# Kernel optimization log

Measured on AMD Instinct MI355X. Metric: run time of the kernel, lower is better.

Reference implementation:

```python
import jax, jax.numpy as jnp
import numpy as np

BN_EPS = 1e-5

def conv1x1(w, b, x):
    # w: [O, C], b: [O], x: [B, C, H, W] -> [B, O, H, W]
    return jnp.einsum('oc,bchw->bohw', w, x) + b[None, :, None, None]

def setup_inputs() -> dict:
    key = jax.random.key(0)
    ks = jax.random.split(key, 11)
    C, inter = 256, 128
    B, H, W = 16, 64, 32
    s = 0.05
    return {
        'x': jax.random.normal(ks[0], (B, C, H, W), jnp.float32),
        'g_w': jax.random.normal(ks[1], (inter, C), jnp.float32) * s,
        'g_b': jax.random.normal(ks[2], (inter,), jnp.float32) * s,
        'theta_w': jax.random.normal(ks[3], (inter, C), jnp.float32) * s,
        'theta_b': jax.random.normal(ks[4], (inter,), jnp.float32) * s,
        'phi_w': jax.random.normal(ks[5], (inter, C), jnp.float32) * s,
        'phi_b': jax.random.normal(ks[6], (inter,), jnp.float32) * s,
        'W_w': jax.random.normal(ks[7], (C, inter), jnp.float32) * s,
        'W_b': jax.random.normal(ks[8], (C,), jnp.float32) * s,
        'bn_gamma': jax.random.normal(ks[9], (C,), jnp.float32) * s,
        'bn_beta': jax.random.normal(ks[10], (C,), jnp.float32) * s,
    }

def reference(x, g_w, g_b, theta_w, theta_b, phi_w, phi_b, W_w, W_b, bn_gamma, bn_beta):
    B, C, H, W = x.shape
    N = H * W
    inter = g_w.shape[0]
    # 1x1 conv projections, flattened to token sequences
    g_x = conv1x1(g_w, g_b, x).reshape(B, inter, N).transpose(0, 2, 1)        # [B, N, inter]
    theta_x = conv1x1(theta_w, theta_b, x).reshape(B, inter, N).transpose(0, 2, 1)  # [B, N, inter]
    phi_x = conv1x1(phi_w, phi_b, x).reshape(B, inter, N)                      # [B, inter, N]
    # non-local attention: f = theta @ phi / N, then y = f @ g
    f_div_c = jnp.einsum('bnd,bdm->bnm', theta_x, phi_x) / N                   # [B, N, N]
    y = jnp.einsum('bnm,bmd->bnd', f_div_c, g_x)                               # [B, N, inter]
    y = y.transpose(0, 2, 1).reshape(B, inter, H, W)
    # W: 1x1 conv + BatchNorm (training-mode batch statistics)
    z = conv1x1(W_w, W_b, y)                                                   # [B, C, H, W]
    mean = jnp.mean(z, axis=(0, 2, 3), keepdims=True)
    var = jnp.var(z, axis=(0, 2, 3), keepdims=True)
    z_hat = (z - mean) * jax.lax.rsqrt(var + BN_EPS)
    z_bn = z_hat * bn_gamma[None, :, None, None] + bn_beta[None, :, None, None]
    return z_bn + x
```

## Files before the change

kernel.cpp:

```cpp
#include <hip/hip_runtime.h>

typedef unsigned int uint;
typedef unsigned short ushort;
typedef __attribute__((ext_vector_type(8))) short bf16x8;
typedef __attribute__((ext_vector_type(4))) float f32x4;

#define BB 16
#define CC 256
#define II 128
#define NN 2048
#define BN_EPS 1e-5f

#define OFF_GPART 0
#define OFF_SPART 8388608
#define OFF_CP    8421376
#define OFF_STATP 8425472
#define OFF_STAT2 8556544
#define OFF_PT    8557056
#define OFF_R1    8557312
#define OFF_WGB   8557568
#define OFF_ALPHA 8557824
#define OFF_L1    8558080
#define OFF_R2    8562176
#define OFF_FEND  8566272
#define UGRAM 0
#define UE    1048576
#define UFT   1114112
#define USBF  1179648
#define UXT   2228224
#define UZ    10616832

static __device__ __forceinline__ ushort f2bf(float f) {
    uint u = __float_as_uint(f);
    return (ushort)((u + 0x7FFFu + ((u >> 16) & 1u)) >> 16);
}
static __device__ __forceinline__ uint pack2(float a, float b) {
    return (uint)f2bf(a) | ((uint)f2bf(b) << 16);
}
static __device__ __forceinline__ float bflo(uint w) { return __uint_as_float(w << 16); }
static __device__ __forceinline__ float bfhi(uint w) { return __uint_as_float(w & 0xFFFF0000u); }

#define MICRO_FMA(av, bv) \
    acc[0][0] += av.x * bv.x; acc[0][1] += av.x * bv.y; acc[0][2] += av.x * bv.z; acc[0][3] += av.x * bv.w; \
    acc[1][0] += av.y * bv.x; acc[1][1] += av.y * bv.y; acc[1][2] += av.y * bv.z; acc[1][3] += av.y * bv.w; \
    acc[2][0] += av.z * bv.x; acc[2][1] += av.z * bv.y; acc[2][2] += av.z * bv.z; acc[2][3] += av.z * bv.w; \
    acc[3][0] += av.w * bv.x; acc[3][1] += av.w * bv.y; acc[3][2] += av.w * bv.z; acc[3][3] += av.w * bv.w;

__global__ __launch_bounds__(256) void mega1(
    const float* __restrict__ x,
    const float* __restrict__ Ww, const float* __restrict__ Gw,
    const float* __restrict__ Pw, const float* __restrict__ Tw,
    const float* __restrict__ gb, const float* __restrict__ pb, const float* __restrict__ tb,
    float* __restrict__ gpart, float* __restrict__ sPart, ushort* __restrict__ xT,
    ushort* __restrict__ EBF, ushort* __restrict__ FT,
    float* __restrict__ pt, float* __restrict__ r1, float* __restrict__ wgb,
    float* __restrict__ alpha)
{
    __shared__ __align__(16) char smem[20480];
    const int bid = blockIdx.x;
    const int t = threadIdx.x;

    if (bid < 512) {
        ushort (*As)[40] = (ushort(*)[40])smem;
        ushort (*Bs)[40] = (ushort(*)[40])(smem + 10240);
        const int jt = bid & 1, it = (bid >> 1) & 1;
        const int z = bid >> 2;
        const int b = z >> 3, kc = z & 7;
        const int iBase = it * 128, jBase = jt * 128;
        const bool diag = (it == jt);
        const int arow = t >> 1, ah = t & 1;
        const float* aSrc = x + ((size_t)(b * CC + iBase + arow)) * NN + kc * 256 + ah * 16;
        const float* bSrc = x + ((size_t)(b * CC + jBase + arow)) * NN + kc * 256 + ah * 16;
        const int lane = t & 63, wid = t >> 6;
        const int mb = (wid >> 1) * 64, nb = (wid & 1) * 64;
        const int lm = lane & 15, q = lane >> 4;
        f32x4 acc[4][4] = {};
        float ssum = 0.f;

        for (int it16 = 0; it16 < 8; ++it16) {
            const float4* ap = (const float4*)(aSrc + it16 * 32);
            float4 a0 = ap[0], a1 = ap[1], a2 = ap[2], a3 = ap[3];
            uint4 pa0 = { pack2(a0.x,a0.y), pack2(a0.z,a0.w), pack2(a1.x,a1.y), pack2(a1.z,a1.w) };
            uint4 pa1 = { pack2(a2.x,a2.y), pack2(a2.z,a2.w), pack2(a3.x,a3.y), pack2(a3.z,a3.w) };
            *(uint4*)&As[arow][ah * 16]     = pa0;
            *(uint4*)&As[arow][ah * 16 + 8] = pa1;
            if (!diag) {
                const float4* bp = (const float4*)(bSrc + it16 * 32);
                float4 b0 = bp[0], b1 = bp[1], b2 = bp[2], b3 = bp[3];
                uint4 pb0 = { pack2(b0.x,b0.y), pack2(b0.z,b0.w), pack2(b1.x,b1.y), pack2(b1.z,b1.w) };
                uint4 pb1 = { pack2(b2.x,b2.y), pack2(b2.z,b2.w), pack2(b3.x,b3.y), pack2(b3.z,b3.w) };
                *(uint4*)&Bs[arow][ah * 16]     = pb0;
                *(uint4*)&Bs[arow][ah * 16 + 8] = pb1;
            }
            if (jt == 0) {
                ssum += a0.x+a0.y+a0.z+a0.w + a1.x+a1.y+a1.z+a1.w
                      + a2.x+a2.y+a2.z+a2.w + a3.x+a3.y+a3.z+a3.w;
            }
            __syncthreads();
            const ushort (*Bsel)[40] = diag ? (const ushort(*)[40])As : (const ushort(*)[40])Bs;
            bf16x8 af[4], bf[4];
            #pragma unroll
            for (int mt = 0; mt < 4; ++mt)
                af[mt] = *(const bf16x8*)&As[mb + mt * 16 + lm][q * 8];
            #pragma unroll
            for (int nt = 0; nt < 4; ++nt)
                bf[nt] = *(const bf16x8*)&Bsel[nb + nt * 16 + lm][q * 8];
            #pragma unroll
            for (int mt = 0; mt < 4; ++mt)
                #pragma unroll
                for (int nt = 0; nt < 4; ++nt)
                    acc[mt][nt] = __builtin_amdgcn_mfma_f32_16x16x32_bf16(af[mt], bf[nt], acc[mt][nt], 0, 0, 0);
            if (diag) {
                const int n_l = t & 31, cg = t >> 5;
                uint qv[8];
                #pragma unroll
                for (int i2 = 0; i2 < 8; ++i2) {
                    ushort lo = As[cg * 16 + 2*i2][n_l];
                    ushort hi = As[cg * 16 + 2*i2 + 1][n_l];
                    qv[i2] = (uint)lo | ((uint)hi << 16);
                }
                const int ng = kc * 256 + it16 * 32 + n_l;
                uint4* op = (uint4*)(xT + ((size_t)(b * NN + ng)) * CC + iBase + cg * 16);
                op[0] = make_uint4(qv[0], qv[1], qv[2], qv[3]);
                op[1] = make_uint4(qv[4], qv[5], qv[6], qv[7]);
            }
            __syncthreads();
        }
        float* gp = gpart + ((size_t)kc * BB + b) * CC * CC;
        #pragma unroll
        for (int mt = 0; mt < 4; ++mt)
            #pragma unroll
            for (int nt = 0; nt < 4; ++nt)
                #pragma unroll
                for (int r = 0; r < 4; ++r) {
                    const int gi = iBase + mb + mt * 16 + q * 4 + r;
                    const int gj = jBase + nb + nt * 16 + lm;
                    gp[(size_t)gi * CC + gj] = acc[mt][nt][r];
                }
        if (jt == 0) {
            const float so = __shfl_xor(ssum, 1);
            if ((t & 1) == 0)
                sPart[((size_t)kc * BB + b) * CC + iBase + arow] = ssum + so;
        }
        return;
    }

    const int bz = bid - 512;
    if (bz == 32) {
        float ptv = 0.f, r1v = 0.f, wgbv = 0.f;
        for (int d = 0; d < II; ++d) {
            ptv  += Pw[(size_t)d * CC + t] * tb[d];
            r1v  += Tw[(size_t)d * CC + t] * pb[d];
            wgbv += Ww[(size_t)t * II + d] * gb[d];
        }
        pt[t] = ptv; r1[t] = r1v; wgb[t] = wgbv;
        if (t == 0) {
            float al = 0.f;
            for (int d = 0; d < II; ++d) al += pb[d] * tb[d];
            alpha[0] = al;
        }
        return;
    }
    float (*As)[68] = (float(*)[68])smem;
    float (*Bs)[68] = (float(*)[68])(smem + 8704);
    const int a_r = t >> 2, a_k = (t & 3) * 8;
    const int b_n = t & 63, b_k = t >> 6;
    const int ty = t >> 4, tx = t & 15;
    float acc[4][4] = {};
    if (bz < 16) {
        const int cBase = (bz >> 2) * 64, iBase = (bz & 3) * 64;
        const float* ap0 = Ww + (size_t)(cBase + a_r) * II + a_k;
        const float* bp0 = Gw + iBase + b_n;
        for (int k0 = 0; k0 < II; k0 += 32) {
            #pragma unroll
            for (int j = 0; j < 8; ++j) As[a_k + j][a_r] = ap0[k0 + j];
            #pragma unroll
            for (int kk = 0; kk < 8; ++kk) {
                const int k = b_k + kk * 4;
                Bs[k][b_n] = bp0[(size_t)(k0 + k) * CC];
            }
            __syncthreads();
            #pragma unroll
            for (int k = 0; k < 32; ++k) {
                const float4 av = *(const float4*)&As[k][ty * 4];
                const float4 bv = *(const float4*)&Bs[k][tx * 4];
                MICRO_FMA(av, bv)
            }
            __syncthreads();
        }
        #pragma unroll
        for (int ii = 0; ii < 4; ++ii) {
            uint2 o = { pack2(acc[ii][0], acc[ii][1]), pack2(acc[ii][2], acc[ii][3]) };
            *(uint2*)&EBF[(size_t)(cBase + ty * 4 + ii) * CC + iBase + tx * 4] = o;
        }
    } else {
        const int zz = bz - 16;
        const int jBase = (zz >> 2) * 64, kBase = (zz & 3) * 64;
        const float* ap0 = Tw + jBase + b_n;
        const float* bp0 = Pw + kBase + b_n;
        for (int k0 = 0; k0 < II; k0 += 32) {
            #pragma unroll
            for (int kk = 0; kk < 8; ++kk) {
                const int k = b_k + kk * 4;
                As[k][b_n] = ap0[(size_t)(k0 + k) * CC];
                Bs[k][b_n] = bp0[(size_t)(k0 + k) * CC];
            }
            __syncthreads();
            #pragma unroll
            for (int k = 0; k < 32; ++k) {
                const float4 av = *(const float4*)&As[k][ty * 4];
                const float4 bv = *(const float4*)&Bs[k][tx * 4];
                MICRO_FMA(av, bv)
            }
            __syncthreads();
        }
        const float sc = 1.0f / (float)NN;
        #pragma unroll
        for (int ii = 0; ii < 4; ++ii) {
            uint2 o = { pack2(acc[ii][0]*sc, acc[ii][1]*sc), pack2(acc[ii][2]*sc, acc[ii][3]*sc) };
            *(uint2*)&FT[(size_t)(jBase + ty * 4 + ii) * CC + kBase + tx * 4] = o;
        }
    }
}

__global__ __launch_bounds__(256) void mega2(
    const float* __restrict__ gpart, const float* __restrict__ sPart,
    const ushort* __restrict__ EBF, const ushort* __restrict__ FT,
    const float* __restrict__ pt, const float* __restrict__ r1,
    const float* __restrict__ wgb, const float* __restrict__ alpha,
    ushort* __restrict__ GramBF,
    float* __restrict__ cprime, float* __restrict__ L1, float* __restrict__ R2)
{
    const int bid = blockIdx.x;
    const int t = threadIdx.x;
    if (bid < 1024) {
        const int i = bid * 256 + t;
        const size_t S = (size_t)BB * CC * CC / 4;
        const float4* p = (const float4*)gpart;
        float4 o = { 0.f, 0.f, 0.f, 0.f };
        #pragma unroll
        for (int k = 0; k < 8; ++k) {
            float4 v = p[i + (size_t)k * S];
            o.x += v.x; o.y += v.y; o.z += v.z; o.w += v.w;
        }
        uint2 pk = { pack2(o.x, o.y), pack2(o.z, o.w) };
        ((uint2*)GramBF)[i] = pk;
        return;
    }
    const int b = bid - 1024;
    __shared__ __align__(16) float sL[256], ptL[256], GptL[256], red[256];
    {
        float s = 0.f;
        #pragma unroll
        for (int kc = 0; kc < 8; ++kc) s += sPart[((size_t)kc * BB + b) * CC + t];
        sL[t] = s;
        ptL[t] = pt[t];
    }
    __syncthreads();
    red[t] = sL[t] * ptL[t];
    __syncthreads();
    for (int s = 128; s > 0; s >>= 1) {
        if (t < s) red[t] += red[t + s];
        __syncthreads();
    }
    const float spt = red[0];
    const int lane = t & 63, wv = t >> 6;
    {
        const float4 pt4 = *(const float4*)&ptL[lane * 4];
        for (int r = wv; r < 256; r += 4) {
            float a = 0.f;
            #pragma unroll
            for (int kc = 0; kc < 8; ++kc) {
                const float4 g = *(const float4*)&gpart[(((size_t)kc * BB + b) * CC + r) * CC + lane * 4];
                a += g.x * pt4.x + g.y * pt4.y + g.z * pt4.z + g.w * pt4.w;
            }
            #pragma unroll
            for (int m = 32; m > 0; m >>= 1) a += __shfl_xor(a, m);
            if (lane == 0) GptL[r] = a;
        }
    }
    __syncthreads();
    float es = 0.f, eg = 0.f;
    {
        const uint4* ep = (const uint4*)(EBF + (size_t)t * CC);
        #pragma unroll 4
        for (int kk = 0; kk < 32; ++kk) {
            uint4 v = ep[kk]; const int k = kk * 8;
            float e0=bflo(v.x),e1=bfhi(v.x),e2=bflo(v.y),e3=bfhi(v.y);
            float e4=bflo(v.z),e5=bfhi(v.z),e6=bflo(v.w),e7=bfhi(v.w);
            es += e0*sL[k]+e1*sL[k+1]+e2*sL[k+2]+e3*sL[k+3]+e4*sL[k+4]+e5*sL[k+5]+e6*sL[k+6]+e7*sL[k+7];
            eg += e0*GptL[k]+e1*GptL[k+1]+e2*GptL[k+2]+e3*GptL[k+3]+e4*GptL[k+4]+e5*GptL[k+5]+e6*GptL[k+6]+e7*GptL[k+7];
        }
    }
    float r2 = 0.f;
    {
        const uint4* fp = (const uint4*)(FT + (size_t)t * CC);
        #pragma unroll 4
        for (int kk = 0; kk < 32; ++kk) {
            uint4 v = fp[kk]; const int k = kk * 8;
            r2 += bflo(v.x)*sL[k]   + bfhi(v.x)*sL[k+1] + bflo(v.y)*sL[k+2] + bfhi(v.y)*sL[k+3]
                + bflo(v.z)*sL[k+4] + bfhi(v.z)*sL[k+5] + bflo(v.w)*sL[k+6] + bfhi(v.w)*sL[k+7];
        }
    }
    const float al = alpha[0];
    const float wg = wgb[t];
    cprime[b * CC + t] = (eg + al * es + spt * wg) / (float)NN + al * wg;
    L1[b * CC + t] = es / (float)NN;
    R2[b * CC + t] = r2 + r1[t];
}

__global__ __launch_bounds__(256) void sfused(
    const ushort* __restrict__ EBF, const ushort* __restrict__ GramBF,
    const ushort* __restrict__ FT,
    const float* __restrict__ r1, const float* __restrict__ R2,
    const float* __restrict__ L1, const float* __restrict__ wgb,
    ushort* __restrict__ Sbf)
{
    __shared__ ushort As[128][40];
    __shared__ ushort Bs[128][40];
    __shared__ ushort Qs[128][264];
    const int t = threadIdx.x;
    const int b = blockIdx.x >> 2;
    const int ct = (blockIdx.x >> 1) & 1, jt = blockIdx.x & 1;
    const int cBase = ct * 128, jBase = jt * 128;
    const int arow = t >> 1, ah = t & 1;
    const int lane = t & 63, wid = t >> 6;
    const int mb = (wid >> 1) * 64, nb = (wid & 1) * 64;
    const int lm = lane & 15, q = lane >> 4;
    const ushort* aSrc = EBF + (size_t)(cBase + arow) * CC + ah * 16;

    #pragma unroll
    for (int half = 0; half < 2; ++half) {
        const ushort* bSrc = GramBF + ((size_t)b * CC + half * 128 + arow) * CC + ah * 16;
        f32x4 acc[4][4] = {};
        for (int k0 = 0; k0 < CC; k0 += 32) {
            *(uint4*)&As[arow][ah * 16]     = ((const uint4*)(aSrc + k0))[0];
            *(uint4*)&As[arow][ah * 16 + 8] = ((const uint4*)(aSrc + k0))[1];
            *(uint4*)&Bs[arow][ah * 16]     = ((const uint4*)(bSrc + k0))[0];
            *(uint4*)&Bs[arow][ah * 16 + 8] = ((const uint4*)(bSrc + k0))[1];
            __syncthreads();
            bf16x8 af[4], bf[4];
            #pragma unroll
            for (int mt = 0; mt < 4; ++mt)
                af[mt] = *(const bf16x8*)&As[mb + mt * 16 + lm][q * 8];
            #pragma unroll
            for (int nt = 0; nt < 4; ++nt)
                bf[nt] = *(const bf16x8*)&Bs[nb + nt * 16 + lm][q * 8];
            #pragma unroll
            for (int mt = 0; mt < 4; ++mt)
                #pragma unroll
                for (int nt = 0; nt < 4; ++nt)
                    acc[mt][nt] = __builtin_amdgcn_mfma_f32_16x16x32_bf16(af[mt], bf[nt], acc[mt][nt], 0, 0, 0);
            __syncthreads();
        }
        #pragma unroll
        for (int mt = 0; mt < 4; ++mt)
            #pragma unroll
            for (int nt = 0; nt < 4; ++nt)
                #pragma unroll
                for (int r = 0; r < 4; ++r)
                    Qs[mb + mt * 16 + q * 4 + r][half * 128 + nb + nt * 16 + lm] = f2bf(acc[mt][nt][r]);
        __syncthreads();
    }
    f32x4 acc[4][4] = {};
    const ushort* fSrc = FT + (size_t)(jBase + arow) * CC + ah * 16;
    for (int k0 = 0; k0 < CC; k0 += 32) {
        *(uint4*)&Bs[arow][ah * 16]     = ((const uint4*)(fSrc + k0))[0];
        *(uint4*)&Bs[arow][ah * 16 + 8] = ((const uint4*)(fSrc + k0))[1];
        __syncthreads();
        bf16x8 af[4], bf[4];
        #pragma unroll
        for (int mt = 0; mt < 4; ++mt)
            af[mt] = *(const bf16x8*)&Qs[mb + mt * 16 + lm][k0 + q * 8];
        #pragma unroll
        for (int nt = 0; nt < 4; ++nt)
            bf[nt] = *(const bf16x8*)&Bs[nb + nt * 16 + lm][q * 8];
        #pragma unroll
        for (int mt = 0; mt < 4; ++mt)
            #pragma unroll
            for (int nt = 0; nt < 4; ++nt)
                acc[mt][nt] = __builtin_amdgcn_mfma_f32_16x16x32_bf16(af[mt], bf[nt], acc[mt][nt], 0, 0, 0);
        __syncthreads();
    }
    float r1v[4], R2v[4];
    #pragma unroll
    for (int nt = 0; nt < 4; ++nt) {
        const int j = jBase + nb + nt * 16 + lm;
        r1v[nt] = r1[j];
        R2v[nt] = R2[b * CC + j];
    }
    ushort* dst = Sbf + (size_t)b * CC * CC;
    #pragma unroll
    for (int mt = 0; mt < 4; ++mt)
        #pragma unroll
        for (int r = 0; r < 4; ++r) {
            const int c = cBase + mb + mt * 16 + q * 4 + r;
            const float l1v = L1[b * CC + c], wgv = wgb[c];
            #pragma unroll
            for (int nt = 0; nt < 4; ++nt) {
                const int j = jBase + nb + nt * 16 + lm;
                dst[(size_t)c * CC + j] = f2bf(acc[mt][nt][r] + l1v * r1v[nt] + wgv * R2v[nt]);
            }
        }
}

__global__ __launch_bounds__(256) void z_mfma(
    const ushort* __restrict__ Sbf, const ushort* __restrict__ xT,
    const float* __restrict__ cprime, ushort* __restrict__ zbf,
    float* __restrict__ statsPart)
{
    __shared__ ushort As[128][40];
    __shared__ ushort Bs[128][40];
    __shared__ float cpL[128];
    __shared__ float sSum[2][128], sSq[2][128];
    const int t = threadIdx.x;
    const int n0 = blockIdx.x * 128, ct = blockIdx.y * 128, b = blockIdx.z;
    const int arow = t >> 1, ah = t & 1;
    const ushort* aSrc = Sbf + ((size_t)(b * CC + ct + arow)) * CC + ah * 16;
    const ushort* bSrc = xT + ((size_t)(b * NN + n0 + arow)) * CC + ah * 16;
    const int lane = t & 63, wid = t >> 6;
    const int mb = (wid >> 1) * 64, nb = (wid & 1) * 64;
    const int lm = lane & 15, q = lane >> 4;
    f32x4 acc[4][4] = {};

    if (t < 128) cpL[t] = cprime[b * CC + ct + t];

    for (int k0 = 0; k0 < CC; k0 += 32) {
        *(uint4*)&As[arow][ah * 16]     = ((const uint4*)(aSrc + k0))[0];
        *(uint4*)&As[arow][ah * 16 + 8] = ((const uint4*)(aSrc + k0))[1];
        *(uint4*)&Bs[arow][ah * 16]     = ((const uint4*)(bSrc + k0))[0];
        *(uint4*)&Bs[arow][ah * 16 + 8] = ((const uint4*)(bSrc + k0))[1];
        __syncthreads();
        bf16x8 af[4], bf[4];
        #pragma unroll
        for (int mt = 0; mt < 4; ++mt)
            af[mt] = *(const bf16x8*)&As[mb + mt * 16 + lm][q * 8];
        #pragma unroll
        for (int nt = 0; nt < 4; ++nt)
            bf[nt] = *(const bf16x8*)&Bs[nb + nt * 16 + lm][q * 8];
        #pragma unroll
        for (int mt = 0; mt < 4; ++mt)
            #pragma unroll
            for (int nt = 0; nt < 4; ++nt)
                acc[mt][nt] = __builtin_amdgcn_mfma_f32_16x16x32_bf16(af[mt], bf[nt], acc[mt][nt], 0, 0, 0);
        __syncthreads();
    }
    const int nbw = wid & 1;
    #pragma unroll
    for (int mt = 0; mt < 4; ++mt) {
        #pragma unroll
        for (int r = 0; r < 4; ++r) {
            const int cl = mb + mt * 16 + q * 4 + r;
            const int ci = ct + cl;
            const float cp = cpL[cl];
            const size_t zrow = ((size_t)(b * CC + ci)) * NN;
            float s1 = 0.f, q1 = 0.f;
            #pragma unroll
            for (int nt = 0; nt < 4; ++nt) {
                const float val = acc[mt][nt][r] + cp;
                const int tok = n0 + nb + nt * 16 + lm;
                zbf[zrow + tok] = f2bf(val);
                s1 += val; q1 += val * val;
            }
            #pragma unroll
            for (int m = 1; m < 16; m <<= 1) {
                s1 += __shfl_xor(s1, m);
                q1 += __shfl_xor(q1, m);
            }
            if (lm == 0) { sSum[nbw][cl] = s1; sSq[nbw][cl] = q1; }
        }
    }
    __syncthreads();
    if (t < 128) {
        const int slot = blockIdx.z * 16 + blockIdx.x;
        statsPart[(size_t)slot * 512 + ct + t]       = sSum[0][t] + sSum[1][t];
        statsPart[(size_t)slot * 512 + 256 + ct + t] = sSq[0][t] + sSq[1][t];
    }
}

__global__ __launch_bounds__(512) void bn_finalize(
    const float* __restrict__ statsPart, float* __restrict__ stats2)
{
    __shared__ float red[4][128];
    __shared__ float sf[128];
    const int g = blockIdx.x;
    const int t = threadIdx.x;
    const int cl = t & 127, sg = t >> 7;
    const int col = (cl < 64) ? (g * 64 + cl) : (256 + g * 64 + (cl - 64));
    float a = 0.f;
    for (int s = sg * 64; s < sg * 64 + 64; ++s)
        a += statsPart[(size_t)s * 512 + col];
    red[sg][cl] = a;
    __syncthreads();
    if (t < 128) sf[t] = red[0][t] + red[1][t] + red[2][t] + red[3][t];
    __syncthreads();
    if (t < 64) {
        const float cnt = (float)(BB * NN);
        const float mean = sf[t] / cnt;
        const float var = sf[64 + t] / cnt - mean * mean;
        const int c = g * 64 + t;
        stats2[c] = mean;
        stats2[CC + c] = rsqrtf(var + BN_EPS);
    }
}

__global__ __launch_bounds__(256) void bn_apply(
    const ushort* __restrict__ zbf, const float* __restrict__ x,
    float* __restrict__ out, const float* __restrict__ stats2,
    const float* __restrict__ gamma, const float* __restrict__ beta)
{
    const size_t i = (size_t)blockIdx.x * 256 + threadIdx.x;
    const size_t base = i * 8;
    const int c = (int)((base >> 11) & (CC - 1));
    const float mean = stats2[c], istd = stats2[CC + c];
    const float gm = gamma[c] * istd;
    const float bt = beta[c] - mean * gm;
    const uint4 zz = *(const uint4*)(zbf + base);
    const float4 x0 = *(const float4*)(x + base);
    const float4 x1 = *(const float4*)(x + base + 4);
    float4 o0, o1;
    o0.x = bflo(zz.x) * gm + bt + x0.x;  o0.y = bfhi(zz.x) * gm + bt + x0.y;
    o0.z = bflo(zz.y) * gm + bt + x0.z;  o0.w = bfhi(zz.y) * gm + bt + x0.w;
    o1.x = bflo(zz.z) * gm + bt + x1.x;  o1.y = bfhi(zz.z) * gm + bt + x1.y;
    o1.z = bflo(zz.w) * gm + bt + x1.z;  o1.w = bfhi(zz.w) * gm + bt + x1.w;
    *(float4*)(out + base) = o0;
    *(float4*)(out + base + 4) = o1;
}

extern "C" void kernel_launch(void* const* d_in, const int* in_sizes, int n_in,
                              void* d_out, int out_size, void* d_ws, size_t ws_size,
                              hipStream_t stream) {
    const float* x    = (const float*)d_in[0];
    const float* g_w  = (const float*)d_in[1];
    const float* g_b  = (const float*)d_in[2];
    const float* th_w = (const float*)d_in[3];
    const float* th_b = (const float*)d_in[4];
    const float* ph_w = (const float*)d_in[5];
    const float* ph_b = (const float*)d_in[6];
    const float* W_w  = (const float*)d_in[7];
    const float* bn_g = (const float*)d_in[9];
    const float* bn_bt= (const float*)d_in[10];
    float* wsf = (float*)d_ws;
    float* out = (float*)d_out;
    ushort* ub = (ushort*)(wsf + OFF_FEND);

    mega1<<<dim3(545), 256, 0, stream>>>(
        x, W_w, g_w, ph_w, th_w, g_b, ph_b, th_b,
        wsf + OFF_GPART, wsf + OFF_SPART, ub + UXT,
        ub + UE, ub + UFT,
        wsf + OFF_PT, wsf + OFF_R1, wsf + OFF_WGB, wsf + OFF_ALPHA);
    mega2<<<dim3(1040), 256, 0, stream>>>(
        wsf + OFF_GPART, wsf + OFF_SPART, ub + UE, ub + UFT,
        wsf + OFF_PT, wsf + OFF_R1, wsf + OFF_WGB, wsf + OFF_ALPHA,
        ub + UGRAM, wsf + OFF_CP, wsf + OFF_L1, wsf + OFF_R2);
    sfused<<<dim3(64), 256, 0, stream>>>(
        ub + UE, ub + UGRAM, ub + UFT,
        wsf + OFF_R1, wsf + OFF_R2, wsf + OFF_L1, wsf + OFF_WGB, ub + USBF);
    z_mfma<<<dim3(16, 2, 16), 256, 0, stream>>>(
        ub + USBF, ub + UXT, wsf + OFF_CP, ub + UZ, wsf + OFF_STATP);
    bn_finalize<<<dim3(4), 512, 0, stream>>>(wsf + OFF_STATP, wsf + OFF_STAT2);
    bn_apply<<<dim3(4096), 256, 0, stream>>>(ub + UZ, x, out, wsf + OFF_STAT2, bn_g, bn_bt);
}
```

Measured before the change: 231.1 us.

## Halve Gram split-K chunks and compute G·pt during partial reduction

The Gram-matrix stage now splits the N dimension into 4 chunks of 512 instead of 8 of 256. Each block runs twice as many K iterations, and the partial-Gram workspace shrinks by half. The reduction kernel now sums 4 partials and also computes the Gram·pt row dot products, writing them to a new Gpt buffer. A separate small u_kernel reads that buffer instead of re-reading all partials per batch. This cuts partial-Gram traffic and redundant reads, at the cost of fewer blocks in the first kernel (256 vs 512) and an extra kernel launch.

Measured after the change: 190.4 us. -17.6%, faster.

```diff
diff --git a/kernel.cpp b/kernel.cpp
--- a/kernel.cpp
+++ b/kernel.cpp
@@ -12,17 +12,18 @@
 #define BN_EPS 1e-5f
 
 #define OFF_GPART 0
-#define OFF_SPART 8388608
-#define OFF_CP    8421376
-#define OFF_STATP 8425472
-#define OFF_STAT2 8556544
-#define OFF_PT    8557056
-#define OFF_R1    8557312
-#define OFF_WGB   8557568
-#define OFF_ALPHA 8557824
-#define OFF_L1    8558080
-#define OFF_R2    8562176
-#define OFF_FEND  8566272
+#define OFF_SPART 4194304
+#define OFF_GPT   4210688
+#define OFF_CP    4214784
+#define OFF_STATP 4218880
+#define OFF_STAT2 4349952
+#define OFF_PT    4350464
+#define OFF_R1    4350720
+#define OFF_WGB   4350976
+#define OFF_ALPHA 4351232
+#define OFF_L1    4351488
+#define OFF_R2    4355584
+#define OFF_FEND  4359680
 #define UGRAM 0
 #define UE    1048576
 #define UFT   1114112
@@ -60,24 +61,24 @@
     const int bid = blockIdx.x;
     const int t = threadIdx.x;
 
-    if (bid < 512) {
+    if (bid < 256) {
         ushort (*As)[40] = (ushort(*)[40])smem;
         ushort (*Bs)[40] = (ushort(*)[40])(smem + 10240);
         const int jt = bid & 1, it = (bid >> 1) & 1;
         const int z = bid >> 2;
-        const int b = z >> 3, kc = z & 7;
+        const int b = z >> 2, kc = z & 3;
         const int iBase = it * 128, jBase = jt * 128;
         const bool diag = (it == jt);
         const int arow = t >> 1, ah = t & 1;
-        const float* aSrc = x + ((size_t)(b * CC + iBase + arow)) * NN + kc * 256 + ah * 16;
-        const float* bSrc = x + ((size_t)(b * CC + jBase + arow)) * NN + kc * 256 + ah * 16;
+        const float* aSrc = x + ((size_t)(b * CC + iBase + arow)) * NN + kc * 512 + ah * 16;
+        const float* bSrc = x + ((size_t)(b * CC + jBase + arow)) * NN + kc * 512 + ah * 16;
         const int lane = t & 63, wid = t >> 6;
         const int mb = (wid >> 1) * 64, nb = (wid & 1) * 64;
         const int lm = lane & 15, q = lane >> 4;
         f32x4 acc[4][4] = {};
         float ssum = 0.f;
 
-        for (int it16 = 0; it16 < 8; ++it16) {
+        for (int it16 = 0; it16 < 16; ++it16) {
             const float4* ap = (const float4*)(aSrc + it16 * 32);
             float4 a0 = ap[0], a1 = ap[1], a2 = ap[2], a3 = ap[3];
             uint4 pa0 = { pack2(a0.x,a0.y), pack2(a0.z,a0.w), pack2(a1.x,a1.y), pack2(a1.z,a1.w) };
@@ -119,7 +120,7 @@
                     ushort hi = As[cg * 16 + 2*i2 + 1][n_l];
                     qv[i2] = (uint)lo | ((uint)hi << 16);
                 }
-                const int ng = kc * 256 + it16 * 32 + n_l;
+                const int ng = kc * 512 + it16 * 32 + n_l;
                 uint4* op = (uint4*)(xT + ((size_t)(b * NN + ng)) * CC + iBase + cg * 16);
                 op[0] = make_uint4(qv[0], qv[1], qv[2], qv[3]);
                 op[1] = make_uint4(qv[4], qv[5], qv[6], qv[7]);
@@ -145,7 +146,7 @@
         return;
     }
 
-    const int bz = bid - 512;
+    const int bz = bid - 256;
     if (bz == 32) {
         float ptv = 0.f, r1v = 0.f, wgbv = 0.f;
         for (int d = 0; d < II; ++d) {
@@ -224,62 +225,56 @@
 }
 
 __global__ __launch_bounds__(256) void mega2(
-    const float* __restrict__ gpart, const float* __restrict__ sPart,
+    const float* __restrict__ gpart, const float* __restrict__ pt,
+    ushort* __restrict__ GramBF, float* __restrict__ Gpt)
+{
+    __shared__ float ptL[256];
+    const int bid = blockIdx.x;
+    const int t = threadIdx.x;
+    const int i = bid * 256 + t;
+    const size_t S = (size_t)BB * CC * CC / 4;
+    const float4* p = (const float4*)gpart;
+    float4 v0 = p[i], v1 = p[i + S], v2 = p[i + 2 * S], v3 = p[i + 3 * S];
+    if (t < 256) ptL[t] = pt[t];
+    float4 o = { v0.x + v1.x + v2.x + v3.x, v0.y + v1.y + v2.y + v3.y,
+                 v0.z + v1.z + v2.z + v3.z, v0.w + v1.w + v2.w + v3.w };
+    uint2 pk = { pack2(o.x, o.y), pack2(o.z, o.w) };
+    ((uint2*)GramBF)[i] = pk;
+    __syncthreads();
+    const int lane = t & 63;
+    float dot = o.x * ptL[lane * 4] + o.y * ptL[lane * 4 + 1]
+              + o.z * ptL[lane * 4 + 2] + o.w * ptL[lane * 4 + 3];
+    #pragma unroll
+    for (int m = 32; m > 0; m >>= 1) dot += __shfl_xor(dot, m);
+    if (lane == 0) {
+        const int row = bid * 4 + (t >> 6);
+        Gpt[row] = dot;
+    }
+}
+
+__global__ __launch_bounds__(256) void u_kernel(
+    const float* __restrict__ sPart, const float* __restrict__ Gpt,
     const ushort* __restrict__ EBF, const ushort* __restrict__ FT,
     const float* __restrict__ pt, const float* __restrict__ r1,
     const float* __restrict__ wgb, const float* __restrict__ alpha,
-    ushort* __restrict__ GramBF,
     float* __restrict__ cprime, float* __restrict__ L1, float* __restrict__ R2)
 {
-    const int bid = blockIdx.x;
-    const int t = threadIdx.x;
-    if (bid < 1024) {
-        const int i = bid * 256 + t;
-        const size_t S = (size_t)BB * CC * CC / 4;
-        const float4* p = (const float4*)gpart;
-        float4 o = { 0.f, 0.f, 0.f, 0.f };
-        #pragma unroll
-        for (int k = 0; k < 8; ++k) {
-            float4 v = p[i + (size_t)k * S];
-            o.x += v.x; o.y += v.y; o.z += v.z; o.w += v.w;
-        }
-        uint2 pk = { pack2(o.x, o.y), pack2(o.z, o.w) };
-        ((uint2*)GramBF)[i] = pk;
-        return;
-    }
-    const int b = bid - 1024;
-    __shared__ __align__(16) float sL[256], ptL[256], GptL[256], red[256];
+    const int b = blockIdx.x, t = threadIdx.x;
+    __shared__ __align__(16) float sL[256], GptL[256], red[256];
     {
         float s = 0.f;
         #pragma unroll
-        for (int kc = 0; kc < 8; ++kc) s += sPart[((size_t)kc * BB + b) * CC + t];
+        for (int kc = 0; kc < 4; ++kc) s += sPart[((size_t)kc * BB + b) * CC + t];
         sL[t] = s;
-        ptL[t] = pt[t];
-    }
-    __syncthreads();
-    red[t] = sL[t] * ptL[t];
+        GptL[t] = Gpt[b * CC + t];
+        red[t] = s * pt[t];
+    }
     __syncthreads();
     for (int s = 128; s > 0; s >>= 1) {
         if (t < s) red[t] += red[t + s];
         __syncthreads();
     }
     const float spt = red[0];
-    const int lane = t & 63, wv = t >> 6;
-    {
-        const float4 pt4 = *(const float4*)&ptL[lane * 4];
-        for (int r = wv; r < 256; r += 4) {
-            float a = 0.f;
-            #pragma unroll
-            for (int kc = 0; kc < 8; ++kc) {
-                const float4 g = *(const float4*)&gpart[(((size_t)kc * BB + b) * CC + r) * CC + lane * 4];
-                a += g.x * pt4.x + g.y * pt4.y + g.z * pt4.z + g.w * pt4.w;
-            }
-            #pragma unroll
-            for (int m = 32; m > 0; m >>= 1) a += __shfl_xor(a, m);
-            if (lane == 0) GptL[r] = a;
-        }
-    }
-    __syncthreads();
     float es = 0.f, eg = 0.f;
     {
         const uint4* ep = (const uint4*)(EBF + (size_t)t * CC);
@@ -544,15 +539,17 @@
     float* out = (float*)d_out;
     ushort* ub = (ushort*)(wsf + OFF_FEND);
 
-    mega1<<<dim3(545), 256, 0, stream>>>(
+    mega1<<<dim3(289), 256, 0, stream>>>(
         x, W_w, g_w, ph_w, th_w, g_b, ph_b, th_b,
         wsf + OFF_GPART, wsf + OFF_SPART, ub + UXT,
         ub + UE, ub + UFT,
         wsf + OFF_PT, wsf + OFF_R1, wsf + OFF_WGB, wsf + OFF_ALPHA);
-    mega2<<<dim3(1040), 256, 0, stream>>>(
-        wsf + OFF_GPART, wsf + OFF_SPART, ub + UE, ub + UFT,
+    mega2<<<dim3(1024), 256, 0, stream>>>(
+        wsf + OFF_GPART, wsf + OFF_PT, ub + UGRAM, wsf + OFF_GPT);
+    u_kernel<<<dim3(16), 256, 0, stream>>>(
+        wsf + OFF_SPART, wsf + OFF_GPT, ub + UE, ub + UFT,
         wsf + OFF_PT, wsf + OFF_R1, wsf + OFF_WGB, wsf + OFF_ALPHA,
-        ub + UGRAM, wsf + OFF_CP, wsf + OFF_L1, wsf + OFF_R2);
+        wsf + OFF_CP, wsf + OFF_L1, wsf + OFF_R2);
     sfused<<<dim3(64), 256, 0, stream>>>(
         ub + UE, ub + UGRAM, ub + UFT,
         wsf + OFF_R1, wsf + OFF_R2, wsf + OFF_L1, wsf + OFF_WGB, ub + USBF);
```
